# Performance work log

Hardware: AMD Instinct MI355X
Metric: run time of the kernel (lower is better)

## Reference

```python
import jax, jax.numpy as jnp
import numpy as np


def setup_inputs() -> dict:
    key = jax.random.key(0)
    B, C, A, P, N = 4, 1, 180, 384, 256
    sinogram = jax.random.normal(key, (B, C, A, P), dtype=jnp.float32)
    # projection angles uniformly covering [0, pi)
    thetas = jnp.linspace(0.0, np.pi, A, endpoint=False).astype(jnp.float32)
    # uniformly spaced detector positions centered at 0, unit spacing
    positions = jnp.arange(P, dtype=jnp.float32) - (P - 1) / 2.0
    return {"sinogram": sinogram, "thetas": thetas, "positions": positions, "image_size": N}


def reference(sinogram, thetas, positions, image_size):
    """Radon backprojection: image[y,x] = sum_a interp(sinogram[a], x*cos+y*sin)."""
    B, C, A, P = sinogram.shape
    N = image_size
    # pixel-center coordinates, image centered at origin (y axis pointing up)
    c = jnp.arange(N, dtype=sinogram.dtype) - (N - 1) / 2.0
    xs = c[None, :]          # [1, N]
    ys = -c[:, None]         # [N, 1]
    cos = jnp.cos(thetas)[:, None, None]  # [A, 1, 1]
    sin = jnp.sin(thetas)[:, None, None]
    t = xs[None] * cos + ys[None] * sin   # [A, N, N] detector coordinate per (angle, pixel)
    # fractional index into the (uniform) detector position grid
    dp = positions[1] - positions[0]
    f = (t - positions[0]) / dp           # [A, N, N]
    i0 = jnp.floor(f)
    w = f - i0                            # linear interpolation weight
    valid = (i0 >= 0) & (i0 <= P - 2)     # rays falling inside the detector
    i0c = jnp.clip(i0, 0, P - 2).astype(jnp.int32)
    idx = i0c.reshape(A, N * N)[None, None]          # [1, 1, A, N*N]
    v0 = jnp.take_along_axis(sinogram, idx, axis=3)  # [B, C, A, N*N]
    v1 = jnp.take_along_axis(sinogram, idx + 1, axis=3)
    wf = w.reshape(A, N * N)[None, None]
    vm = valid.reshape(A, N * N)[None, None]
    val = jnp.where(vm, v0 * (1.0 - wf) + v1 * wf, 0.0)
    return val.sum(axis=2).reshape(B, C, N, N)
```

## Files before the change

### kernel.cpp

```cpp
#include <hip/hip_runtime.h>
#include <cmath>


template <int BATCH>
__global__ __launch_bounds__(256) void radon_partial_lds(
    const float* __restrict__ sino,
    const float* __restrict__ thetas,
    const float* __restrict__ positions,
    float* __restrict__ part,
    int A, int P, int N, int chunk)
{
    constexpr int MAXP = 512;
    __shared__ float s_cs[256];
    __shared__ float s_sn[256];
    __shared__ float buf[2][BATCH * MAXP];

    const int tid = threadIdx.x;
    const float p0     = positions[0];
    const float inv_dp = 1.0f / (positions[1] - p0);
    if (tid < A) {
        float th = thetas[tid];
        s_cs[tid] = cosf(th) * inv_dp;
        s_sn[tid] = sinf(th) * inv_dp;
    }

    const int nn    = N * N;
    const int pix   = blockIdx.x * blockDim.x + tid;
    const int a0    = blockIdx.y * chunk;
    const int cnt   = min(A, a0 + chunk) - a0;
    const int bstride = A * P;
    const int halfP = P >> 1;

    const int x = pix % N;
    const int y = pix / N;
    const float half = (float)(N - 1) * 0.5f;
    const float cx = (float)x - half;
    const float cy = half - (float)y;
    const float q0 = -p0 * inv_dp;

    float acc[BATCH];
#pragma unroll
    for (int b = 0; b < BATCH; ++b) acc[b] = 0.0f;

    if (tid < halfP) {
#pragma unroll
        for (int b = 0; b < BATCH; ++b) {
            float2 v = *(const float2*)(sino + (size_t)b * bstride
                                             + (size_t)a0 * P + 2 * tid);
            *(float2*)(&buf[0][b * P + 2 * tid]) = v;
        }
    }
    __syncthreads();

    for (int i = 0; i < cnt; ++i) {
        const int cur = i & 1;
        if (i + 1 < cnt && tid < halfP) {
            const int an = a0 + i + 1;
#pragma unroll
            for (int b = 0; b < BATCH; ++b) {
                float2 v = *(const float2*)(sino + (size_t)b * bstride
                                                 + (size_t)an * P + 2 * tid);
                *(float2*)(&buf[cur ^ 1][b * P + 2 * tid]) = v;
            }
        }

        const int a = a0 + i;
        float f   = fmaf(cx, s_cs[a], fmaf(cy, s_sn[a], q0));
        float i0f = floorf(f);
        int   i0  = (int)i0f;
        float w   = f - i0f;
        float m   = (i0 >= 0 && i0 <= P - 2) ? 1.0f : 0.0f;
        int   ic  = min(max(i0, 0), P - 2);
        const float* bp = &buf[cur][ic];
#pragma unroll
        for (int b = 0; b < BATCH; ++b) {
            float v0 = bp[b * P];
            float v1 = bp[b * P + 1];
            acc[b] = fmaf(m, fmaf(w, v1 - v0, v0), acc[b]);
        }
        __syncthreads();
    }

    if (pix < nn) {
        float* pp = part + ((size_t)blockIdx.y * BATCH) * nn + pix;
#pragma unroll
        for (int b = 0; b < BATCH; ++b) pp[(size_t)b * nn] = acc[b];
    }
}

__global__ __launch_bounds__(256) void radon_reduce_kernel(
    const float4* __restrict__ part,
    float4* __restrict__ out,
    int BN4, int nchunks)
{
    int i = blockIdx.x * blockDim.x + threadIdx.x;
    if (i >= BN4) return;
    float4 s = make_float4(0.f, 0.f, 0.f, 0.f);
    for (int c = 0; c < nchunks; ++c) {
        float4 v = part[(size_t)c * BN4 + i];
        s.x += v.x; s.y += v.y; s.z += v.z; s.w += v.w;
    }
    out[i] = s;
}

__global__ __launch_bounds__(256) void radon_direct_kernel(
    const float* __restrict__ sino,
    const float* __restrict__ thetas,
    const float* __restrict__ positions,
    float* __restrict__ out,
    int A, int P, int N, int BC)
{
    const int nn  = N * N;
    const int pix = blockIdx.x * blockDim.x + threadIdx.x;
    if (pix >= nn) return;
    const float p0     = positions[0];
    const float inv_dp = 1.0f / (positions[1] - p0);
    const int x = pix % N;
    const int y = pix / N;
    const float half = (float)(N - 1) * 0.5f;
    const float cx = (float)x - half;
    const float cy = half - (float)y;
    for (int b = 0; b < BC; ++b) {
        float acc = 0.0f;
        for (int a = 0; a < A; ++a) {
            float th = thetas[a];
            float f  = (cx * cosf(th) + cy * sinf(th) - p0) * inv_dp;
            float i0f = floorf(f);
            int i0 = (int)i0f;
            float w = f - i0f;
            float m = (i0 >= 0 && i0 <= P - 2) ? 1.0f : 0.0f;
            int ic = min(max(i0, 0), P - 2);
            const float* row = sino + ((size_t)b * A + a) * P + ic;
            acc = fmaf(m, fmaf(w, row[1] - row[0], row[0]), acc);
        }
        out[(size_t)b * nn + pix] = acc;
    }
}

extern "C" void kernel_launch(void* const* d_in, const int* in_sizes, int n_in,
                              void* d_out, int out_size, void* d_ws, size_t ws_size,
                              hipStream_t stream) {
    const float* sino      = (const float*)d_in[0];
    const float* thetas    = (const float*)d_in[1];
    const float* positions = (const float*)d_in[2];
    float* out             = (float*)d_out;

    const int A  = in_sizes[1];
    const int P  = in_sizes[2];
    const int BC = in_sizes[0] / (A * P);
    const int N  = (int)lroundf(sqrtf((float)(out_size / BC)));
    const int nn = N * N;

    const int ACHUNKS = 8;
    const int chunk   = (A + ACHUNKS - 1) / ACHUNKS;
    const size_t need = (size_t)ACHUNKS * BC * nn * sizeof(float);

    const bool fast = (BC == 4) && (A <= 256) && (P <= 512) && ((P & 1) == 0)
                   && (ws_size >= need) && ((nn & 255) == 0) && ((nn & 3) == 0);

    if (fast) {
        float* part = (float*)d_ws;
        dim3 block(256);
        dim3 grid1(nn / 256, ACHUNKS);
        radon_partial_lds<4><<<grid1, block, 0, stream>>>(
            sino, thetas, positions, part, A, P, N, chunk);
        const int BN4 = BC * nn / 4;
        dim3 grid2((BN4 + 255) / 256);
        radon_reduce_kernel<<<grid2, block, 0, stream>>>(
            (const float4*)part, (float4*)out, BN4, ACHUNKS);
    } else {
        dim3 block(256);
        dim3 grid((nn + 255) / 256);
        radon_direct_kernel<<<grid, block, 0, stream>>>(
            sino, thetas, positions, out, A, P, N, BC);
    }
}
```

Measured before the change: 83.97 us.

## Pack sinogram into fp16 pairs per detector bin and stage via direct LDS loads

Adds a pre-pass that converts the sinogram to half precision and interleaves, for each angle and detector bin, the neighbouring bin value and all four batch entries into one 16-byte element. It also precomputes scaled trig values. The backprojection kernel then does one 16-byte LDS read per angle instead of eight scalar reads, and stages rows with global_load_lds async copies. The costs are an extra kernel launch, a workspace round trip for the packed data, and fp16 rounding of the sinogram values, which may exceed the accuracy tolerance.

```diff
diff --git a/kernel.cpp b/kernel.cpp
--- a/kernel.cpp
+++ b/kernel.cpp
@@ -1,91 +1,120 @@
 #include <hip/hip_runtime.h>
+#include <hip/hip_fp16.h>
 #include <cmath>
 
 
-template <int BATCH>
-__global__ __launch_bounds__(256) void radon_partial_lds(
+#define ACHUNKS 8
+#define MAXPE   512
+
+__device__ __forceinline__ void stage_pe(const uint4* __restrict__ g,
+                                         uint4* l, int PE, int tid)
+{
+    for (int e = tid; e < PE; e += 256) {
+        const int wb = e & ~63;
+        uint32_t lds_off = (uint32_t)(uintptr_t)(l + wb);
+        __builtin_amdgcn_global_load_lds(
+            (const __attribute__((address_space(1))) uint32_t*)(g + e),
+            (__attribute__((address_space(3))) uint32_t*)(uintptr_t)lds_off,
+            16, 0, 0);
+    }
+}
+
+__global__ __launch_bounds__(256) void radon_pack(
     const float* __restrict__ sino,
     const float* __restrict__ thetas,
     const float* __restrict__ positions,
-    float* __restrict__ part,
-    int A, int P, int N, int chunk)
-{
-    constexpr int MAXP = 512;
-    __shared__ float s_cs[256];
-    __shared__ float s_sn[256];
-    __shared__ float buf[2][BATCH * MAXP];
-
-    const int tid = threadIdx.x;
+    uint4* __restrict__ packed,
+    float2* __restrict__ trig,
+    int A, int P, int PE, int bstride)
+{
+    const int idx = blockIdx.x * 256 + threadIdx.x;
+    const int a = idx / PE;
+    const int i = idx - a * PE;
+    if (a >= A) return;
+
     const float p0     = positions[0];
     const float inv_dp = 1.0f / (positions[1] - p0);
-    if (tid < A) {
-        float th = thetas[tid];
-        s_cs[tid] = cosf(th) * inv_dp;
-        s_sn[tid] = sinf(th) * inv_dp;
-    }
-
-    const int nn    = N * N;
-    const int pix   = blockIdx.x * blockDim.x + tid;
-    const int a0    = blockIdx.y * chunk;
-    const int cnt   = min(A, a0 + chunk) - a0;
-    const int bstride = A * P;
-    const int halfP = P >> 1;
+    if (i == 0) {
+        float th = thetas[a];
+        trig[a] = make_float2(cosf(th) * inv_dp, sinf(th) * inv_dp);
+        if (a == 0) trig[A] = make_float2(-p0 * inv_dp, 0.0f);
+    }
+
+    const int i0 = min(i, P - 1);
+    const int i1 = min(i + 1, P - 1);
+    const float* s = sino + (size_t)a * P;
+
+    uint4 e;
+    unsigned* ep = (unsigned*)&e;
+#pragma unroll
+    for (int b = 0; b < 4; ++b) {
+        const float* sb = s + (size_t)b * bstride;
+        __half2 h = __floats2half2_rn(sb[i0], sb[i1]);
+        ep[b] = *(const unsigned*)&h;
+    }
+    packed[(size_t)a * PE + i] = e;
+}
+
+__global__ __launch_bounds__(256) void radon_partial_pk(
+    const uint4* __restrict__ packed,
+    const float2* __restrict__ trig,
+    float* __restrict__ part,
+    int A, int P, int PE, int N, int chunk)
+{
+    __shared__ uint4 buf[2][MAXPE];
+
+    const int tid = threadIdx.x;
+    const int nn  = N * N;
+    const int pix = blockIdx.x * 256 + tid;
+    const int a0  = blockIdx.y * chunk;
+    const int cnt = min(A, a0 + chunk) - a0;
 
     const int x = pix % N;
     const int y = pix / N;
     const float half = (float)(N - 1) * 0.5f;
     const float cx = (float)x - half;
     const float cy = half - (float)y;
-    const float q0 = -p0 * inv_dp;
-
-    float acc[BATCH];
-#pragma unroll
-    for (int b = 0; b < BATCH; ++b) acc[b] = 0.0f;
-
-    if (tid < halfP) {
-#pragma unroll
-        for (int b = 0; b < BATCH; ++b) {
-            float2 v = *(const float2*)(sino + (size_t)b * bstride
-                                             + (size_t)a0 * P + 2 * tid);
-            *(float2*)(&buf[0][b * P + 2 * tid]) = v;
-        }
-    }
+    const float q0 = trig[A].x;
+
+    float acc0 = 0.f, acc1 = 0.f, acc2 = 0.f, acc3 = 0.f;
+
+    stage_pe(packed + (size_t)a0 * PE, &buf[0][0], PE, tid);
     __syncthreads();
 
     for (int i = 0; i < cnt; ++i) {
         const int cur = i & 1;
-        if (i + 1 < cnt && tid < halfP) {
-            const int an = a0 + i + 1;
-#pragma unroll
-            for (int b = 0; b < BATCH; ++b) {
-                float2 v = *(const float2*)(sino + (size_t)b * bstride
-                                                 + (size_t)an * P + 2 * tid);
-                *(float2*)(&buf[cur ^ 1][b * P + 2 * tid]) = v;
-            }
-        }
-
-        const int a = a0 + i;
-        float f   = fmaf(cx, s_cs[a], fmaf(cy, s_sn[a], q0));
+        if (i + 1 < cnt)
+            stage_pe(packed + (size_t)(a0 + i + 1) * PE, &buf[cur ^ 1][0], PE, tid);
+
+        float2 t  = trig[a0 + i];
+        float f   = fmaf(cx, t.x, fmaf(cy, t.y, q0));
         float i0f = floorf(f);
         int   i0  = (int)i0f;
         float w   = f - i0f;
         float m   = (i0 >= 0 && i0 <= P - 2) ? 1.0f : 0.0f;
         int   ic  = min(max(i0, 0), P - 2);
-        const float* bp = &buf[cur][ic];
-#pragma unroll
-        for (int b = 0; b < BATCH; ++b) {
-            float v0 = bp[b * P];
-            float v1 = bp[b * P + 1];
-            acc[b] = fmaf(m, fmaf(w, v1 - v0, v0), acc[b]);
-        }
+        float wm  = w * m;
+        float om  = m - wm;
+
+        uint4 e = buf[cur][ic];
+        const __half2* hp = (const __half2*)&e;
+        float2 g0 = __half22float2(hp[0]);
+        float2 g1 = __half22float2(hp[1]);
+        float2 g2 = __half22float2(hp[2]);
+        float2 g3 = __half22float2(hp[3]);
+        acc0 = fmaf(om, g0.x, fmaf(wm, g0.y, acc0));
+        acc1 = fmaf(om, g1.x, fmaf(wm, g1.y, acc1));
+        acc2 = fmaf(om, g2.x, fmaf(wm, g2.y, acc2));
+        acc3 = fmaf(om, g3.x, fmaf(wm, g3.y, acc3));
+
         __syncthreads();
     }
 
-    if (pix < nn) {
-        float* pp = part + ((size_t)blockIdx.y * BATCH) * nn + pix;
-#pragma unroll
-        for (int b = 0; b < BATCH; ++b) pp[(size_t)b * nn] = acc[b];
-    }
+    float* pp = part + (size_t)blockIdx.y * 4 * nn + pix;
+    pp[0]              = acc0;
+    pp[(size_t)nn]     = acc1;
+    pp[(size_t)2 * nn] = acc2;
+    pp[(size_t)3 * nn] = acc3;
 }
 
 __global__ __launch_bounds__(256) void radon_reduce_kernel(
@@ -150,23 +179,36 @@
     const int BC = in_sizes[0] / (A * P);
     const int N  = (int)lroundf(sqrtf((float)(out_size / BC)));
     const int nn = N * N;
-
-    const int ACHUNKS = 8;
-    const int chunk   = (A + ACHUNKS - 1) / ACHUNKS;
-    const size_t need = (size_t)ACHUNKS * BC * nn * sizeof(float);
-
-    const bool fast = (BC == 4) && (A <= 256) && (P <= 512) && ((P & 1) == 0)
-                   && (ws_size >= need) && ((nn & 255) == 0) && ((nn & 3) == 0);
+    const int bstride = A * P;
+
+    const int PE    = (P + 63) & ~63;
+    const int chunk = (A + ACHUNKS - 1) / ACHUNKS;
+
+    const size_t part_bytes   = (size_t)ACHUNKS * 4 * nn * sizeof(float);
+    const size_t packed_bytes = (size_t)A * PE * sizeof(uint4);
+    const size_t trig_bytes   = (size_t)(A + 1) * sizeof(float2);
+    const size_t need = part_bytes + packed_bytes + trig_bytes;
+
+    const bool fast = (BC == 4) && (A <= 256) && (P >= 2) && (PE <= MAXPE)
+                   && (N % 64 == 0) && ((nn & 255) == 0) && (ws_size >= need);
 
     if (fast) {
-        float* part = (float*)d_ws;
+        float*  part   = (float*)d_ws;
+        uint4*  packed = (uint4*)((char*)d_ws + part_bytes);
+        float2* trig   = (float2*)((char*)d_ws + part_bytes + packed_bytes);
+
         dim3 block(256);
-        dim3 grid1(nn / 256, ACHUNKS);
-        radon_partial_lds<4><<<grid1, block, 0, stream>>>(
-            sino, thetas, positions, part, A, P, N, chunk);
-        const int BN4 = BC * nn / 4;
-        dim3 grid2((BN4 + 255) / 256);
-        radon_reduce_kernel<<<grid2, block, 0, stream>>>(
+        dim3 gpack(((unsigned)(A * PE) + 255) / 256);
+        radon_pack<<<gpack, block, 0, stream>>>(
+            sino, thetas, positions, packed, trig, A, P, PE, bstride);
+
+        dim3 gpart(nn / 256, ACHUNKS);
+        radon_partial_pk<<<gpart, block, 0, stream>>>(
+            packed, trig, part, A, P, PE, N, chunk);
+
+        const int BN4 = 4 * nn / 4;
+        dim3 gred((BN4 + 255) / 256);
+        radon_reduce_kernel<<<gred, block, 0, stream>>>(
             (const float4*)part, (float4*)out, BN4, ACHUNKS);
     } else {
         dim3 block(256);
```

New measurement: 83.98 us. About the same (+0.0%).
